# Kernel optimization log

Hardware: AMD Instinct MI355X
Metric: run time of the kernel (lower is better)

The kernel has to match this reference:

```python
import jax, jax.numpy as jnp
import numpy as np

SEQ, D_IN, D_OUT, RANK, N_ADAPTERS = 8192, 4096, 4096, 16, 8


def setup_inputs() -> dict:
    key = jax.random.key(0)
    ks = jax.random.split(key, 7)
    return {
        "x": jax.random.normal(ks[0], (SEQ, D_IN), jnp.float32),
        "weight": jax.random.normal(ks[1], (D_IN, D_OUT), jnp.float32) * (D_IN ** -0.5),
        "bias": jax.random.normal(ks[2], (D_OUT,), jnp.float32),
        "A_buffer": jax.random.normal(ks[3], (N_ADAPTERS, RANK, D_IN), jnp.float32) * (D_IN ** -0.5),
        "B_buffer": jax.random.normal(ks[4], (N_ADAPTERS, D_OUT, RANK), jnp.float32) * (RANK ** -0.5),
        "scalings": jax.random.uniform(ks[5], (SEQ,), jnp.float32, 0.5, 2.0),
        "token_indices": jax.random.randint(ks[6], (SEQ,), 0, N_ADAPTERS, jnp.int32),
    }


def reference(x, weight, bias, A_buffer, B_buffer, scalings, token_indices):
    # Base linear layer: [S, D_in] @ [D_in, D_out] + bias
    base_output = x @ weight + bias
    n_adapters = A_buffer.shape[0]
    delta = jnp.zeros_like(base_output)
    # Grouped LoRA GEMM: per-adapter small GEMMs, masked scatter back per token.
    for e in range(n_adapters):
        # run_lora_a_gemm: x @ A[e]^T with per-token scaling -> [S, rank]
        a_out = (x @ A_buffer[e].T) * scalings[:, None]
        # run_lora_b_gemm: a_out @ B[e]^T -> [S, D_out]
        b_out = a_out @ B_buffer[e].T
        delta = delta + jnp.where((token_indices == e)[:, None], b_out, 0.0)
    return base_output + delta
```

## Files before the change

kernel.cpp:

```cpp
#include <hip/hip_runtime.h>
#include <hip/hip_bf16.h>
#include <cstdint>

#define SEQ   8192
#define DIN   4096
#define DOUT  4096
#define RANK  16
#define NAD   8
#define KC    (DIN + NAD*RANK)

using f32x4  = __attribute__((ext_vector_type(4))) float;
using bf16x8 = __attribute__((ext_vector_type(8))) short;

__device__ __forceinline__ unsigned short f2bf(float f) {
  union { float f; uint32_t u; } v; v.f = f;
  return (unsigned short)((v.u + 0x7fffu + ((v.u >> 16) & 1u)) >> 16);
}

__device__ __forceinline__ void async_copy16(void* lds, const void* gmem) {
  __builtin_amdgcn_global_load_lds(
      (__attribute__((address_space(1))) void*)(uintptr_t)gmem,
      (__attribute__((address_space(3))) void*)(uint32_t)(uintptr_t)lds,
      16, 0, 0);
}


__global__ void cvt_x_kernel(const float* __restrict__ x, unsigned short* __restrict__ xcat) {
  const int64_t nchunks = (int64_t)SEQ * DIN / 8;
  for (int64_t c = (int64_t)blockIdx.x * blockDim.x + threadIdx.x; c < nchunks;
       c += (int64_t)gridDim.x * blockDim.x) {
    int64_t base = c * 8;
    int s = (int)(base >> 12);
    int k = (int)(base & (DIN - 1));
    float4 p = *(const float4*)(x + base);
    float4 q = *(const float4*)(x + base + 4);
    union { unsigned short h[8]; int4 v; } o;
    o.h[0]=f2bf(p.x); o.h[1]=f2bf(p.y); o.h[2]=f2bf(p.z); o.h[3]=f2bf(p.w);
    o.h[4]=f2bf(q.x); o.h[5]=f2bf(q.y); o.h[6]=f2bf(q.z); o.h[7]=f2bf(q.w);
    *(int4*)(xcat + (int64_t)s * KC + k) = o.v;
  }
}

__global__ void cvt_a_kernel(const float* __restrict__ a, unsigned short* __restrict__ abf) {
  int c = blockIdx.x * 256 + threadIdx.x;
  int64_t base = (int64_t)c * 8;
  float4 p = *(const float4*)(a + base);
  float4 q = *(const float4*)(a + base + 4);
  union { unsigned short h[8]; int4 v; } o;
  o.h[0]=f2bf(p.x); o.h[1]=f2bf(p.y); o.h[2]=f2bf(p.z); o.h[3]=f2bf(p.w);
  o.h[4]=f2bf(q.x); o.h[5]=f2bf(q.y); o.h[6]=f2bf(q.z); o.h[7]=f2bf(q.w);
  *(int4*)(abf + base) = o.v;
}

__global__ void cvt_w_kernel(const float* __restrict__ w, unsigned short* __restrict__ wcat) {
  int t  = threadIdx.x;
  int bn = blockIdx.x & 127;
  int bk = blockIdx.x >> 7;
  int n = bn * 32 + (t & 31);
  int k = bk * 64 + (t >> 5) * 8;
  union { unsigned short h[8]; int4 v; } o;
#pragma unroll
  for (int j = 0; j < 8; j++)
    o.h[j] = f2bf(w[(int64_t)(k + j) * DOUT + n]);
  *(int4*)(wcat + (int64_t)n * KC + k) = o.v;
}

__global__ void cvt_b_kernel(const float* __restrict__ Bbuf, unsigned short* __restrict__ wcat) {
  int idx = blockIdx.x * 256 + threadIdx.x;
  int n = idx >> 7, er = idx & 127;
  int e = er >> 4, r = er & 15;
  float v = Bbuf[((int64_t)e * DOUT + n) * RANK + r];
  wcat[(int64_t)n * KC + DIN + er] = f2bf(v);
}

__global__ __launch_bounds__(256) void gemm_lora_a(
    const unsigned short* __restrict__ A,
    const unsigned short* __restrict__ Bb,
    float* __restrict__ aout) {
  constexpr int BK = 64;
  __shared__ unsigned short sA[64 * BK];
  __shared__ unsigned short sB[128 * BK];
  int tid = threadIdx.x, wave = tid >> 6, lane = tid & 63;
  int quad = lane >> 4, l16 = lane & 15;
  int mb = blockIdx.x & 127;
  int sp = blockIdx.x >> 7;
  int row0 = mb * 64;
  int kbase = sp * (DIN / 2);
  int wm = wave >> 1, wn = wave & 1;
  int f8 = l16 & 7;

  const f32x4 zero = {0.f, 0.f, 0.f, 0.f};
  f32x4 acc[2][4];
#pragma unroll
  for (int i = 0; i < 2; i++)
#pragma unroll
    for (int j = 0; j < 4; j++) acc[i][j] = zero;

  for (int kt = 0; kt < (DIN / 2) / BK; ++kt) {
    int k0 = kbase + kt * BK;
#pragma unroll
    for (int i = 0; i < 2; i++) {
      int c = i * 256 + tid;
      int r = c >> 3, kc = ((c & 7) ^ (r & 7)) * 8;
      async_copy16(&sA[c * 8], A + (int64_t)(row0 + r) * KC + k0 + kc);
    }
#pragma unroll
    for (int i = 0; i < 4; i++) {
      int c = i * 256 + tid;
      int r = c >> 3, kc = ((c & 7) ^ (r & 7)) * 8;
      async_copy16(&sB[c * 8], Bb + (int64_t)r * DIN + k0 + kc);
    }
    __syncthreads();
#pragma unroll
    for (int ks = 0; ks < 2; ks++) {
      bf16x8 af[2], bfr[4];
      int qq = ks * 4 + quad;
      int qp = (qq ^ f8) * 8;
#pragma unroll
      for (int mi = 0; mi < 2; mi++)
        af[mi] = *(const bf16x8*)&sA[(wm * 32 + mi * 16 + l16) * BK + qp];
#pragma unroll
      for (int ni = 0; ni < 4; ni++)
        bfr[ni] = *(const bf16x8*)&sB[(wn * 64 + ni * 16 + l16) * BK + qp];
#pragma unroll
      for (int mi = 0; mi < 2; mi++)
#pragma unroll
        for (int ni = 0; ni < 4; ni++)
          acc[mi][ni] = __builtin_amdgcn_mfma_f32_16x16x32_bf16(af[mi], bfr[ni], acc[mi][ni], 0, 0, 0);
    }
    __syncthreads();
  }

  float* op = aout + (int64_t)sp * SEQ * 128;
#pragma unroll
  for (int ni = 0; ni < 4; ni++) {
    int er = wn * 64 + ni * 16 + l16;
#pragma unroll
    for (int mi = 0; mi < 2; mi++) {
      int s0 = row0 + wm * 32 + mi * 16 + quad * 4;
#pragma unroll
      for (int r = 0; r < 4; r++)
        op[(int64_t)(s0 + r) * 128 + er] = acc[mi][ni][r];
    }
  }
}

__global__ void lora_combine(const float* __restrict__ aout, const float* __restrict__ scal,
                             const int* __restrict__ tok, unsigned short* __restrict__ xcat) {
  int idx = blockIdx.x * 256 + threadIdx.x;
  int s = idx >> 7, er = idx & 127;
  float v = aout[idx] + aout[idx + (int64_t)SEQ * 128];
  v *= scal[s];
  v = ((er >> 4) == tok[s]) ? v : 0.0f;
  xcat[(int64_t)s * KC + DIN + er] = f2bf(v);
}


#define CFENCE asm volatile("" ::: "memory")

template<int MQ>
__device__ __forceinline__ void ldsA(const unsigned short* aT, int wm, int l16, int quad,
                                     bf16x8 (&af)[4][2]) {
  int f8 = l16 & 7;
#pragma unroll
  for (int ks = 0; ks < 2; ks++) {
    int qp = ((ks * 4 + quad) ^ f8) * 8;
#pragma unroll
    for (int mi = 0; mi < 4; mi++)
      af[mi][ks] = *(const bf16x8*)&aT[(wm * 128 + MQ * 64 + mi * 16 + l16) * 64 + qp];
  }
}

template<int NQ>
__device__ __forceinline__ void ldsB(const unsigned short* bT, int wn, int l16, int quad,
                                     bf16x8 (&bq)[2][2]) {
  int f8 = l16 & 7;
#pragma unroll
  for (int ks = 0; ks < 2; ks++) {
    int qp = ((ks * 4 + quad) ^ f8) * 8;
#pragma unroll
    for (int ni = 0; ni < 2; ni++)
      bq[ni][ks] = *(const bf16x8*)&bT[(wn * 64 + NQ * 32 + ni * 16 + l16) * 64 + qp];
  }
}

template<int MQ, int NQ>
__device__ __forceinline__ void mfma_quad(f32x4 (&acc)[8][4], bf16x8 (&af)[4][2],
                                          bf16x8 (&bq)[2][2]) {
  __builtin_amdgcn_s_setprio(1);
#pragma unroll
  for (int mi = 0; mi < 4; mi++)
#pragma unroll
    for (int ni = 0; ni < 2; ni++)
#pragma unroll
      for (int ks = 0; ks < 2; ks++)
        acc[MQ * 4 + mi][NQ * 2 + ni] = __builtin_amdgcn_mfma_f32_16x16x32_bf16(
            af[mi][ks], bq[ni][ks], acc[MQ * 4 + mi][NQ * 2 + ni], 0, 0, 0);
  __builtin_amdgcn_s_setprio(0);
}

__device__ __forceinline__ void stage_A(unsigned short* sAb, const unsigned short* Ag,
                                        int mq, int k0, int tid) {
  int rr  = tid >> 3;
  int q8  = (tid & 7) * 8;
  int qc8 = ((tid & 7) ^ (rr & 7)) * 8;
  int r0 = mq * 64 + rr;
  async_copy16(sAb + r0 * 64 + q8, Ag + (int64_t)r0 * KC + k0 + qc8);
  int r1 = r0 + 128;
  async_copy16(sAb + r1 * 64 + q8, Ag + (int64_t)r1 * KC + k0 + qc8);
}

__device__ __forceinline__ void stage_B(unsigned short* sBb, const unsigned short* Bg,
                                        int nq, int k0, int tid) {
  int rB  = ((tid >> 3) & 31) | ((tid >> 8) << 6);
  int q8  = (tid & 7) * 8;
  int qc8 = ((tid & 7) ^ ((tid >> 3) & 7)) * 8;
  int r0 = nq * 32 + rB;
  async_copy16(sBb + r0 * 64 + q8, Bg + (int64_t)r0 * KC + k0 + qc8);
  int r1 = r0 + 128;
  async_copy16(sBb + r1 * 64 + q8, Bg + (int64_t)r1 * KC + k0 + qc8);
}

#define MIDBAR                                                    \
  CFENCE; __builtin_amdgcn_s_barrier();                           \
  asm volatile("s_waitcnt lgkmcnt(0)" ::: "memory")
#define ENDBAR  CFENCE; __builtin_amdgcn_s_barrier(); CFENCE

#define TILE(aT, bT, S0, S1, S2, S3, BND)                         \
  ldsA<0>(aT, wm, l16, quad, af);                                 \
  ldsB<0>(bT, wn, l16, quad, bf0);                                \
  S0; MIDBAR;                                                     \
  mfma_quad<0, 0>(acc, af, bf0);                                  \
  ENDBAR;                                                         \
  ldsB<1>(bT, wn, l16, quad, bf1);                                \
  S1; MIDBAR;                                                     \
  mfma_quad<0, 1>(acc, af, bf1);                                  \
  ENDBAR;                                                         \
  ldsA<1>(aT, wm, l16, quad, af);                                 \
  S2; MIDBAR;                                                     \
  mfma_quad<1, 1>(acc, af, bf1);                                  \
  ENDBAR;                                                         \
  S3; CFENCE;                                                     \
  mfma_quad<1, 0>(acc, af, bf0);                                  \
  BND;                                                            \
  ENDBAR

__global__ __launch_bounds__(512, 2) void gemm_main8(
    const unsigned short* __restrict__ A,
    const unsigned short* __restrict__ B,
    const float* __restrict__ bias,
    float* __restrict__ out) {
  extern __shared__ unsigned short smem[];
  unsigned short* a0 = smem;
  unsigned short* b0 = smem + 16384;
  unsigned short* a1 = smem + 32768;
  unsigned short* b1 = smem + 49152;

  int tid = threadIdx.x, wave = tid >> 6, lane = tid & 63;
  int quad = lane >> 4, l16 = lane & 15;
  int wm = wave >> 2, wn = wave & 3;

  int bid = blockIdx.x;
  int cid = (bid & 7) * 64 + (bid >> 3);
  int bm = cid >> 4, bn = cid & 15;
  int row0 = bm * 256, col0 = bn * 256;

  const unsigned short* Ag = A + (int64_t)row0 * KC;
  const unsigned short* Bg = B + (int64_t)col0 * KC;

  const f32x4 zero = {0.f, 0.f, 0.f, 0.f};
  f32x4 acc[8][4];
#pragma unroll
  for (int i = 0; i < 8; i++)
#pragma unroll
    for (int j = 0; j < 4; j++) acc[i][j] = zero;

  bf16x8 af[4][2], bf0[2][2], bf1[2][2];

  stage_A(a0, Ag, 0, 0, tid);
  stage_B(b0, Bg, 0, 0, tid);
  stage_B(b0, Bg, 1, 0, tid);
  stage_A(a0, Ag, 1, 0, tid);
  stage_A(a1, Ag, 0, 64, tid);
  stage_B(b1, Bg, 1, 64, tid);
  stage_A(a1, Ag, 1, 64, tid);
  asm volatile("s_waitcnt vmcnt(6)" ::: "memory");
  ENDBAR;

#define BND6 asm volatile("s_waitcnt vmcnt(6)" ::: "memory")

  for (int tp = 0; tp < 32; ++tp) {
    int kE = tp * 128;
    TILE(a0, b0,
         stage_B(b1, Bg, 0, kE + 64,  tid),
         stage_A(a0, Ag, 0, kE + 128, tid),
         stage_B(b0, Bg, 1, kE + 128, tid),
         stage_A(a0, Ag, 1, kE + 128, tid),
         BND6);
    TILE(a1, b1,
         stage_B(b0, Bg, 0, kE + 128, tid),
         stage_A(a1, Ag, 0, kE + 192, tid),
         stage_B(b1, Bg, 1, kE + 192, tid),
         stage_A(a1, Ag, 1, kE + 192, tid),
         BND6);
  }

  TILE(a0, b0,
       stage_B(b1, Bg, 0, 4160, tid),
       (void)0, (void)0, (void)0,
       asm volatile("s_waitcnt vmcnt(0)" ::: "memory"));

  ldsA<0>(a1, wm, l16, quad, af);
  ldsB<0>(b1, wn, l16, quad, bf0);
  mfma_quad<0, 0>(acc, af, bf0);
  ldsB<1>(b1, wn, l16, quad, bf1);
  mfma_quad<0, 1>(acc, af, bf1);
  ldsA<1>(a1, wm, l16, quad, af);
  mfma_quad<1, 1>(acc, af, bf1);
  mfma_quad<1, 0>(acc, af, bf0);

#pragma unroll
  for (int ni = 0; ni < 4; ni++) {
    int col = col0 + wn * 64 + ni * 16 + l16;
    float bv = bias[col];
#pragma unroll
    for (int mi = 0; mi < 8; mi++) {
      int rbase = row0 + wm * 128 + mi * 16 + quad * 4;
#pragma unroll
      for (int r = 0; r < 4; r++)
        out[(int64_t)(rbase + r) * DOUT + col] = acc[mi][ni][r] + bv;
    }
  }
}

__global__ void fb_aout(const float* __restrict__ x, const float* __restrict__ Abuf,
                        const float* __restrict__ scal, const int* __restrict__ tok,
                        float* __restrict__ aout) {
  int s = blockIdx.x;
  int e = tok[s];
  __shared__ float red[256];
  for (int r = 0; r < RANK; ++r) {
    float p = 0.f;
    for (int k = threadIdx.x; k < DIN; k += 256)
      p += x[(int64_t)s * DIN + k] * Abuf[((int64_t)e * RANK + r) * DIN + k];
    red[threadIdx.x] = p;
    __syncthreads();
    for (int off = 128; off > 0; off >>= 1) {
      if (threadIdx.x < off) red[threadIdx.x] += red[threadIdx.x + off];
      __syncthreads();
    }
    if (threadIdx.x == 0) aout[s * RANK + r] = red[0] * scal[s];
    __syncthreads();
  }
}
__global__ void fb_out(const float* __restrict__ x, const float* __restrict__ w,
                       const float* __restrict__ bias, const float* __restrict__ Bbuf,
                       const int* __restrict__ tok, const float* __restrict__ aout,
                       float* __restrict__ out) {
  int64_t idx = (int64_t)blockIdx.x * blockDim.x + threadIdx.x;
  int s = (int)(idx >> 12), n = (int)(idx & (DOUT - 1));
  float accv = bias[n];
  for (int k = 0; k < DIN; ++k)
    accv += x[(int64_t)s * DIN + k] * w[(int64_t)k * DOUT + n];
  int e = tok[s];
  float d = 0.f;
  for (int r = 0; r < RANK; ++r)
    d += aout[s * RANK + r] * Bbuf[((int64_t)e * DOUT + n) * RANK + r];
  out[idx] = accv + d;
}

extern "C" void kernel_launch(void* const* d_in, const int* in_sizes, int n_in,
                              void* d_out, int out_size, void* d_ws, size_t ws_size,
                              hipStream_t stream) {
  const float* x    = (const float*)d_in[0];
  const float* w    = (const float*)d_in[1];
  const float* bias = (const float*)d_in[2];
  const float* Abuf = (const float*)d_in[3];
  const float* Bbuf = (const float*)d_in[4];
  const float* scal = (const float*)d_in[5];
  const int*   tok  = (const int*)d_in[6];
  float* out = (float*)d_out;

  const size_t xcat_b = (size_t)SEQ * KC * 2;
  const size_t wcat_b = (size_t)DOUT * KC * 2;
  const size_t abf_b  = (size_t)NAD * RANK * DIN * 2;
  const size_t aout_b = (size_t)2 * SEQ * 128 * 4;

  if (ws_size >= xcat_b + wcat_b + abf_b + aout_b) {
    static bool lds_attr_done = false;
    if (!lds_attr_done) {
      (void)hipFuncSetAttribute((const void*)gemm_main8,
                                hipFuncAttributeMaxDynamicSharedMemorySize, 131072);
      lds_attr_done = true;
    }
    unsigned short* xcat = (unsigned short*)d_ws;
    unsigned short* wcat = (unsigned short*)((char*)d_ws + xcat_b);
    unsigned short* abf  = (unsigned short*)((char*)d_ws + xcat_b + wcat_b);
    float*          aout = (float*)((char*)d_ws + xcat_b + wcat_b + abf_b);
    cvt_x_kernel<<<4096, 256, 0, stream>>>(x, xcat);
    cvt_w_kernel<<<8192, 256, 0, stream>>>(w, wcat);
    cvt_b_kernel<<<(DOUT * 128) / 256, 256, 0, stream>>>(Bbuf, wcat);
    cvt_a_kernel<<<(NAD * RANK * DIN / 8) / 256, 256, 0, stream>>>(Abuf, abf);
    gemm_lora_a<<<256, 256, 0, stream>>>(xcat, abf, aout);
    lora_combine<<<(SEQ * 128) / 256, 256, 0, stream>>>(aout, scal, tok, xcat);
    gemm_main8<<<512, 512, 131072, stream>>>(xcat, wcat, bias, out);
  } else {
    float* aout = (float*)d_ws;
    fb_aout<<<SEQ, 256, 0, stream>>>(x, Abuf, scal, tok, aout);
    fb_out<<<(int)(((int64_t)SEQ * DOUT) / 256), 256, 0, stream>>>(x, w, bias, Bbuf, tok, aout, out);
  }
}
```

Baseline: 546.9 us.

## Merge conversion kernels and fuse LoRA-A scaling/masking into a double-buffered GEMM

Merges the x/A and W/B bf16 conversion kernels into two launches. The LoRA-A GEMM becomes a 16-row-per-block, full-K, double-buffered kernel that applies per-token scaling and adapter masking in its epilogue and writes bf16 straight into the concatenated activation buffer. This removes the split-K fp32 intermediate, the separate combine kernel and three launches. The trade-off is less parallel work per block, since each block now runs a long K loop with small tiles that reload the full A_buffer for every 16 rows.

```diff
diff --git a/kernel.cpp b/kernel.cpp
--- a/kernel.cpp
+++ b/kernel.cpp
@@ -25,134 +25,120 @@
 }
 
 
-__global__ void cvt_x_kernel(const float* __restrict__ x, unsigned short* __restrict__ xcat) {
-  const int64_t nchunks = (int64_t)SEQ * DIN / 8;
-  for (int64_t c = (int64_t)blockIdx.x * blockDim.x + threadIdx.x; c < nchunks;
-       c += (int64_t)gridDim.x * blockDim.x) {
-    int64_t base = c * 8;
-    int s = (int)(base >> 12);
-    int k = (int)(base & (DIN - 1));
-    float4 p = *(const float4*)(x + base);
-    float4 q = *(const float4*)(x + base + 4);
+__global__ void cvt_xa_kernel(const float* __restrict__ x, unsigned short* __restrict__ xcat,
+                              const float* __restrict__ a, unsigned short* __restrict__ abf) {
+  if (blockIdx.x < 4096) {
+    const int64_t nchunks = (int64_t)SEQ * DIN / 8;
+    for (int64_t c = (int64_t)blockIdx.x * 256 + threadIdx.x; c < nchunks;
+         c += (int64_t)4096 * 256) {
+      int64_t base = c * 8;
+      int s = (int)(base >> 12);
+      int k = (int)(base & (DIN - 1));
+      float4 p = *(const float4*)(x + base);
+      float4 q = *(const float4*)(x + base + 4);
+      union { unsigned short h[8]; int4 v; } o;
+      o.h[0]=f2bf(p.x); o.h[1]=f2bf(p.y); o.h[2]=f2bf(p.z); o.h[3]=f2bf(p.w);
+      o.h[4]=f2bf(q.x); o.h[5]=f2bf(q.y); o.h[6]=f2bf(q.z); o.h[7]=f2bf(q.w);
+      *(int4*)(xcat + (int64_t)s * KC + k) = o.v;
+    }
+  } else {
+    int c = (blockIdx.x - 4096) * 256 + threadIdx.x;
+    int64_t base = (int64_t)c * 8;
+    float4 p = *(const float4*)(a + base);
+    float4 q = *(const float4*)(a + base + 4);
     union { unsigned short h[8]; int4 v; } o;
     o.h[0]=f2bf(p.x); o.h[1]=f2bf(p.y); o.h[2]=f2bf(p.z); o.h[3]=f2bf(p.w);
     o.h[4]=f2bf(q.x); o.h[5]=f2bf(q.y); o.h[6]=f2bf(q.z); o.h[7]=f2bf(q.w);
-    *(int4*)(xcat + (int64_t)s * KC + k) = o.v;
-  }
-}
-
-__global__ void cvt_a_kernel(const float* __restrict__ a, unsigned short* __restrict__ abf) {
-  int c = blockIdx.x * 256 + threadIdx.x;
-  int64_t base = (int64_t)c * 8;
-  float4 p = *(const float4*)(a + base);
-  float4 q = *(const float4*)(a + base + 4);
-  union { unsigned short h[8]; int4 v; } o;
-  o.h[0]=f2bf(p.x); o.h[1]=f2bf(p.y); o.h[2]=f2bf(p.z); o.h[3]=f2bf(p.w);
-  o.h[4]=f2bf(q.x); o.h[5]=f2bf(q.y); o.h[6]=f2bf(q.z); o.h[7]=f2bf(q.w);
-  *(int4*)(abf + base) = o.v;
-}
-
-__global__ void cvt_w_kernel(const float* __restrict__ w, unsigned short* __restrict__ wcat) {
-  int t  = threadIdx.x;
-  int bn = blockIdx.x & 127;
-  int bk = blockIdx.x >> 7;
-  int n = bn * 32 + (t & 31);
-  int k = bk * 64 + (t >> 5) * 8;
-  union { unsigned short h[8]; int4 v; } o;
-#pragma unroll
-  for (int j = 0; j < 8; j++)
-    o.h[j] = f2bf(w[(int64_t)(k + j) * DOUT + n]);
-  *(int4*)(wcat + (int64_t)n * KC + k) = o.v;
-}
-
-__global__ void cvt_b_kernel(const float* __restrict__ Bbuf, unsigned short* __restrict__ wcat) {
-  int idx = blockIdx.x * 256 + threadIdx.x;
-  int n = idx >> 7, er = idx & 127;
-  int e = er >> 4, r = er & 15;
-  float v = Bbuf[((int64_t)e * DOUT + n) * RANK + r];
-  wcat[(int64_t)n * KC + DIN + er] = f2bf(v);
-}
-
-__global__ __launch_bounds__(256) void gemm_lora_a(
+    *(int4*)(abf + base) = o.v;
+  }
+}
+
+__global__ void cvt_wb_kernel(const float* __restrict__ w, unsigned short* __restrict__ wcat,
+                              const float* __restrict__ Bbuf) {
+  if (blockIdx.x < 8192) {
+    int t  = threadIdx.x;
+    int bn = blockIdx.x & 127;
+    int bk = blockIdx.x >> 7;
+    int n = bn * 32 + (t & 31);
+    int k = bk * 64 + (t >> 5) * 8;
+    union { unsigned short h[8]; int4 v; } o;
+#pragma unroll
+    for (int j = 0; j < 8; j++)
+      o.h[j] = f2bf(w[(int64_t)(k + j) * DOUT + n]);
+    *(int4*)(wcat + (int64_t)n * KC + k) = o.v;
+  } else {
+    int idx = (blockIdx.x - 8192) * 256 + threadIdx.x;
+    int n = idx >> 7, er = idx & 127;
+    int e = er >> 4, r = er & 15;
+    float v = Bbuf[((int64_t)e * DOUT + n) * RANK + r];
+    wcat[(int64_t)n * KC + DIN + er] = f2bf(v);
+  }
+}
+
+__global__ __launch_bounds__(256) void gemm_lora_a2(
     const unsigned short* __restrict__ A,
     const unsigned short* __restrict__ Bb,
-    float* __restrict__ aout) {
+    const float* __restrict__ scal,
+    const int* __restrict__ tok,
+    unsigned short* __restrict__ xcat) {
   constexpr int BK = 64;
-  __shared__ unsigned short sA[64 * BK];
-  __shared__ unsigned short sB[128 * BK];
+  __shared__ unsigned short sA[2][16 * BK];
+  __shared__ unsigned short sB[2][128 * BK];
   int tid = threadIdx.x, wave = tid >> 6, lane = tid & 63;
   int quad = lane >> 4, l16 = lane & 15;
-  int mb = blockIdx.x & 127;
-  int sp = blockIdx.x >> 7;
-  int row0 = mb * 64;
-  int kbase = sp * (DIN / 2);
-  int wm = wave >> 1, wn = wave & 1;
+  int row0 = blockIdx.x * 16;
   int f8 = l16 & 7;
 
-  const f32x4 zero = {0.f, 0.f, 0.f, 0.f};
-  f32x4 acc[2][4];
-#pragma unroll
-  for (int i = 0; i < 2; i++)
-#pragma unroll
-    for (int j = 0; j < 4; j++) acc[i][j] = zero;
-
-  for (int kt = 0; kt < (DIN / 2) / BK; ++kt) {
-    int k0 = kbase + kt * BK;
-#pragma unroll
-    for (int i = 0; i < 2; i++) {
-      int c = i * 256 + tid;
-      int r = c >> 3, kc = ((c & 7) ^ (r & 7)) * 8;
-      async_copy16(&sA[c * 8], A + (int64_t)(row0 + r) * KC + k0 + kc);
+  f32x4 acc[2];
+  acc[0] = f32x4{0.f, 0.f, 0.f, 0.f};
+  acc[1] = f32x4{0.f, 0.f, 0.f, 0.f};
+
+  auto stage = [&](int b, int kt) {
+    int k0 = kt * BK;
+    if (tid < 128) {
+      int r = tid >> 3, kc = ((tid & 7) ^ (r & 7)) * 8;
+      async_copy16(&sA[b][tid * 8], A + (int64_t)(row0 + r) * KC + k0 + kc);
     }
 #pragma unroll
     for (int i = 0; i < 4; i++) {
       int c = i * 256 + tid;
       int r = c >> 3, kc = ((c & 7) ^ (r & 7)) * 8;
-      async_copy16(&sB[c * 8], Bb + (int64_t)r * DIN + k0 + kc);
+      async_copy16(&sB[b][c * 8], Bb + (int64_t)r * DIN + k0 + kc);
+    }
+  };
+
+  stage(0, 0);
+  __syncthreads();
+
+  for (int kt = 0; kt < DIN / BK; ++kt) {
+    int cur = kt & 1;
+    if (kt + 1 < DIN / BK) stage(cur ^ 1, kt + 1);
+    const unsigned short* sAc = sA[cur];
+    const unsigned short* sBc = sB[cur];
+#pragma unroll
+    for (int ks = 0; ks < 2; ks++) {
+      int qp = ((ks * 4 + quad) ^ f8) * 8;
+      bf16x8 af = *(const bf16x8*)&sAc[l16 * BK + qp];
+      bf16x8 b0 = *(const bf16x8*)&sBc[(wave * 32 + l16) * BK + qp];
+      bf16x8 b1 = *(const bf16x8*)&sBc[(wave * 32 + 16 + l16) * BK + qp];
+      acc[0] = __builtin_amdgcn_mfma_f32_16x16x32_bf16(af, b0, acc[0], 0, 0, 0);
+      acc[1] = __builtin_amdgcn_mfma_f32_16x16x32_bf16(af, b1, acc[1], 0, 0, 0);
     }
     __syncthreads();
-#pragma unroll
-    for (int ks = 0; ks < 2; ks++) {
-      bf16x8 af[2], bfr[4];
-      int qq = ks * 4 + quad;
-      int qp = (qq ^ f8) * 8;
-#pragma unroll
-      for (int mi = 0; mi < 2; mi++)
-        af[mi] = *(const bf16x8*)&sA[(wm * 32 + mi * 16 + l16) * BK + qp];
-#pragma unroll
-      for (int ni = 0; ni < 4; ni++)
-        bfr[ni] = *(const bf16x8*)&sB[(wn * 64 + ni * 16 + l16) * BK + qp];
-#pragma unroll
-      for (int mi = 0; mi < 2; mi++)
-#pragma unroll
-        for (int ni = 0; ni < 4; ni++)
-          acc[mi][ni] = __builtin_amdgcn_mfma_f32_16x16x32_bf16(af[mi], bfr[ni], acc[mi][ni], 0, 0, 0);
-    }
-    __syncthreads();
-  }
-
-  float* op = aout + (int64_t)sp * SEQ * 128;
-#pragma unroll
-  for (int ni = 0; ni < 4; ni++) {
-    int er = wn * 64 + ni * 16 + l16;
-#pragma unroll
-    for (int mi = 0; mi < 2; mi++) {
-      int s0 = row0 + wm * 32 + mi * 16 + quad * 4;
-#pragma unroll
-      for (int r = 0; r < 4; r++)
-        op[(int64_t)(s0 + r) * 128 + er] = acc[mi][ni][r];
-    }
-  }
-}
-
-__global__ void lora_combine(const float* __restrict__ aout, const float* __restrict__ scal,
-                             const int* __restrict__ tok, unsigned short* __restrict__ xcat) {
-  int idx = blockIdx.x * 256 + threadIdx.x;
-  int s = idx >> 7, er = idx & 127;
-  float v = aout[idx] + aout[idx + (int64_t)SEQ * 128];
-  v *= scal[s];
-  v = ((er >> 4) == tok[s]) ? v : 0.0f;
-  xcat[(int64_t)s * KC + DIN + er] = f2bf(v);
+  }
+
+#pragma unroll
+  for (int ni = 0; ni < 2; ni++) {
+    int er = wave * 32 + ni * 16 + l16;
+    int e = er >> 4;
+#pragma unroll
+    for (int r = 0; r < 4; r++) {
+      int s = row0 + quad * 4 + r;
+      float v = acc[ni][r] * scal[s];
+      v = (e == tok[s]) ? v : 0.0f;
+      xcat[(int64_t)s * KC + DIN + er] = f2bf(v);
+    }
+  }
 }
 
 
@@ -384,9 +370,8 @@
   const size_t xcat_b = (size_t)SEQ * KC * 2;
   const size_t wcat_b = (size_t)DOUT * KC * 2;
   const size_t abf_b  = (size_t)NAD * RANK * DIN * 2;
-  const size_t aout_b = (size_t)2 * SEQ * 128 * 4;
-
-  if (ws_size >= xcat_b + wcat_b + abf_b + aout_b) {
+
+  if (ws_size >= xcat_b + wcat_b + abf_b) {
     static bool lds_attr_done = false;
     if (!lds_attr_done) {
       (void)hipFuncSetAttribute((const void*)gemm_main8,
@@ -396,13 +381,9 @@
     unsigned short* xcat = (unsigned short*)d_ws;
     unsigned short* wcat = (unsigned short*)((char*)d_ws + xcat_b);
     unsigned short* abf  = (unsigned short*)((char*)d_ws + xcat_b + wcat_b);
-    float*          aout = (float*)((char*)d_ws + xcat_b + wcat_b + abf_b);
-    cvt_x_kernel<<<4096, 256, 0, stream>>>(x, xcat);
-    cvt_w_kernel<<<8192, 256, 0, stream>>>(w, wcat);
-    cvt_b_kernel<<<(DOUT * 128) / 256, 256, 0, stream>>>(Bbuf, wcat);
-    cvt_a_kernel<<<(NAD * RANK * DIN / 8) / 256, 256, 0, stream>>>(Abuf, abf);
-    gemm_lora_a<<<256, 256, 0, stream>>>(xcat, abf, aout);
-    lora_combine<<<(SEQ * 128) / 256, 256, 0, stream>>>(aout, scal, tok, xcat);
+    cvt_xa_kernel<<<4352, 256, 0, stream>>>(x, xcat, Abuf, abf);
+    cvt_wb_kernel<<<10240, 256, 0, stream>>>(w, wcat, Bbuf);
+    gemm_lora_a2<<<512, 256, 0, stream>>>(xcat, abf, scal, tok, xcat);
     gemm_main8<<<512, 512, 131072, stream>>>(xcat, wcat, bias, out);
   } else {
     float* aout = (float*)d_ws;
```

Result: no change. 551.8 us (+0.9%).
